# Kernel optimization log

Hardware: AMD Instinct MI355X
Metric: run time of the kernel (lower is better)

The kernel has to match this reference:

```python
import jax, jax.numpy as jnp
import numpy as np


def setup_inputs() -> dict:
    key = jax.random.key(0)
    k1, k2, k3, k4 = jax.random.split(key, 4)
    n, L, h = 512, 257, 256
    l = L - 1
    hidden, n_labels = 256, 50
    feat = jax.random.normal(k1, (n, L, h), dtype=jnp.float32)
    heads = jax.random.randint(k2, (n, l), 0, L, dtype=jnp.int64)
    masks = jnp.ones((n, l), dtype=jnp.float32)
    # torch nn.Linear layout: (out_features, in_features); xavier-normal-ish scale
    W1 = jax.random.normal(k3, (hidden, 2 * h), dtype=jnp.float32) * (2.0 / (hidden + 2 * h)) ** 0.5
    b1 = jnp.zeros((hidden,), dtype=jnp.float32)
    W2 = jax.random.normal(k4, (n_labels, hidden), dtype=jnp.float32) * (2.0 / (n_labels + hidden)) ** 0.5
    b2 = jnp.zeros((n_labels,), dtype=jnp.float32)
    return {"feat": feat, "heads": heads, "masks": masks,
            "W1": W1, "b1": b1, "W2": W2, "b2": b2}


def reference(feat, heads, masks, W1, b1, W2, b2):
    # feat: (n, L, h); heads: (n, l) with l = L-1, values in [0, L)
    dependent_f = feat[:, 1:, :]                                   # (n, l, h)
    # head_f[b, i] = feat[b, heads[b, i]]  (the gather)
    head_f = jnp.take_along_axis(feat, heads[:, :, None], axis=1)   # (n, l, h)
    cat_f = jnp.concatenate((dependent_f, head_f), axis=2)          # (n, l, 2h)
    hid = jax.nn.relu(jnp.einsum('nlh,oh->nlo', cat_f, W1) + b1)    # (n, l, hidden); dropout is identity at eval
    label_f = jnp.einsum('nlo,ko->nlk', hid, W2) + b2               # (n, l, n_labels)
    return label_f
```

## Files before the change

kernel.cpp:

```cpp
#include <hip/hip_runtime.h>
#include <hip/hip_bf16.h>
#include <stdint.h>

typedef __bf16 bf16x8 __attribute__((ext_vector_type(8)));
typedef __bf16 bf16x4 __attribute__((ext_vector_type(4)));
typedef float  floatx4 __attribute__((ext_vector_type(4)));

static constexpr int LL   = 257;
static constexpr int HH   = 256;
static constexpr int M    = 131072;
static constexpr int K1   = 512;
static constexpr int NLAB = 50;

__device__ __forceinline__ bf16x8 cvt8(floatx4 a, floatx4 b) {
  bf16x8 v;
  v[0]=(__bf16)a[0]; v[1]=(__bf16)a[1]; v[2]=(__bf16)a[2]; v[3]=(__bf16)a[3];
  v[4]=(__bf16)b[0]; v[5]=(__bf16)b[1]; v[6]=(__bf16)b[2]; v[7]=(__bf16)b[3];
  return v;
}

__global__ void prep_w(const float* __restrict__ W1, const float* __restrict__ W2,
                       __bf16* __restrict__ w1bt, __bf16* __restrict__ w2b) {
  int idx = blockIdx.x * 256 + threadIdx.x;
  if (idx < 16384) {
    int o  = idx >> 6;
    int kc = idx & 63;
    const float4* s = (const float4*)(W1 + (size_t)o * K1 + kc * 8);
    float4 a = s[0], b = s[1];
    bf16x8 v;
    v[0]=(__bf16)a.x; v[1]=(__bf16)a.y; v[2]=(__bf16)a.z; v[3]=(__bf16)a.w;
    v[4]=(__bf16)b.x; v[5]=(__bf16)b.y; v[6]=(__bf16)b.z; v[7]=(__bf16)b.w;
    *(bf16x8*)(w1bt + ((size_t)(kc * 256 + o)) * 8) = v;
  } else {
    int j = idx - 16384;
    int row = j >> 5;
    int col = (j & 31) * 8;
    float4 a = {0.f,0.f,0.f,0.f}, b = {0.f,0.f,0.f,0.f};
    if (row < NLAB) {
      const float4* s = (const float4*)(W2 + (size_t)row * 256 + col);
      a = s[0]; b = s[1];
    }
    bf16x8 v;
    v[0]=(__bf16)a.x; v[1]=(__bf16)a.y; v[2]=(__bf16)a.z; v[3]=(__bf16)a.w;
    v[4]=(__bf16)b.x; v[5]=(__bf16)b.y; v[6]=(__bf16)b.z; v[7]=(__bf16)b.w;
    *(bf16x8*)(w2b + (size_t)j * 8) = v;
  }
}

template<int KT>
__device__ __forceinline__ void kstep(
    bf16x8 (&afc)[4], bf16x8 (&afi)[4], floatx4 (&acc)[4][4],
    const __bf16* afBase, const __bf16* catS, int bbOff) {

  if constexpr (KT < 14) {
    const __bf16* afp = afBase + (KT + 2) * 8192;
    #pragma unroll
    for (int oi = 0; oi < 4; ++oi)
      afi[oi] = *(const bf16x8*)(afp + oi * 128);
  }

  const __bf16* crd = catS + KT * 2048 + bbOff;
  bf16x8 bb[4];
  #pragma unroll
  for (int mi = 0; mi < 4; ++mi)
    bb[mi] = *(const bf16x8*)(crd + mi * 512);
  #pragma unroll
  for (int oi = 0; oi < 4; ++oi)
    #pragma unroll
    for (int mi = 0; mi < 4; ++mi)
      acc[oi][mi] = __builtin_amdgcn_mfma_f32_16x16x32_bf16(afc[oi], bb[mi], acc[oi][mi], 0, 0, 0);
}

__global__ __launch_bounds__(256, 2)
void fused_kernel(const float* __restrict__ feat, const int* __restrict__ heads,
                  const __bf16* __restrict__ w1bt, const float* __restrict__ b1,
                  const __bf16* __restrict__ w2b, const float* __restrict__ b2,
                  float* __restrict__ out) {
  __shared__ __align__(16) char smem[65536];
  __bf16* catS = (__bf16*)smem;
  __bf16* hidS = (__bf16*)smem;

  const int t    = threadIdx.x;
  const int w    = t >> 6;
  const int lane = t & 63;
  const int lr   = lane & 15;
  const int q    = lane >> 4;

  const int mBase = blockIdx.x * 64;

  const int inrow   = t & 7;
  const int rowslot = t >> 3;
  const int seq     = mBase >> 8;
  const int mA      = mBase + rowslot;
  const int mB      = mBase + 32 + rowslot;
  const float* rp[4];
  rp[0] = feat + ((size_t)(seq * LL + (mA & 255) + 1)) * HH + inrow * 8;
  rp[1] = feat + ((size_t)(seq * LL + (mB & 255) + 1)) * HH + inrow * 8;
  rp[2] = feat + ((size_t)(seq * LL + heads[mA])) * HH + inrow * 8;
  rp[3] = feat + ((size_t)(seq * LL + heads[mB])) * HH + inrow * 8;

  #pragma unroll
  for (int g = 0; g < 4; ++g) {
    const int r = (g & 1) * 32 + rowslot;
    const int kbase = (g >= 2) ? 32 : 0;
    #pragma unroll
    for (int s = 0; s < 4; ++s) {
      floatx4 a = *(const floatx4*)(rp[g] + s * 64);
      floatx4 b = *(const floatx4*)(rp[g] + s * 64 + 4);
      const int ko  = kbase + s * 8 + inrow;
      const int kt  = ko >> 2;
      const int c   = ko & 3;
      const int pos = r * 4 + (c ^ ((r >> 1) & 3));
      *(bf16x8*)(catS + kt * 2048 + pos * 8) = cvt8(a, b);
    }
  }

  const int bbOff = lr * 32 + (q ^ ((lr >> 1) & 3)) * 8;
  const __bf16* afBase = w1bt + ((size_t)(q * 256 + w * 64 + lr)) * 8;

  floatx4 acc[4][4];
  #pragma unroll
  for (int i = 0; i < 4; ++i)
    #pragma unroll
    for (int j = 0; j < 4; ++j)
      acc[i][j] = (floatx4){0.f, 0.f, 0.f, 0.f};

  bf16x8 a0[4], a1[4], a2[4];
  #pragma unroll
  for (int oi = 0; oi < 4; ++oi) a0[oi] = *(const bf16x8*)(afBase + oi * 128);
  #pragma unroll
  for (int oi = 0; oi < 4; ++oi) a1[oi] = *(const bf16x8*)(afBase + 8192 + oi * 128);

  __syncthreads();

  kstep< 0>(a0, a2, acc, afBase, catS, bbOff);
  kstep< 1>(a1, a0, acc, afBase, catS, bbOff);
  kstep< 2>(a2, a1, acc, afBase, catS, bbOff);
  kstep< 3>(a0, a2, acc, afBase, catS, bbOff);
  kstep< 4>(a1, a0, acc, afBase, catS, bbOff);
  kstep< 5>(a2, a1, acc, afBase, catS, bbOff);
  kstep< 6>(a0, a2, acc, afBase, catS, bbOff);
  kstep< 7>(a1, a0, acc, afBase, catS, bbOff);
  kstep< 8>(a2, a1, acc, afBase, catS, bbOff);
  kstep< 9>(a0, a2, acc, afBase, catS, bbOff);
  kstep<10>(a1, a0, acc, afBase, catS, bbOff);
  kstep<11>(a2, a1, acc, afBase, catS, bbOff);
  kstep<12>(a0, a2, acc, afBase, catS, bbOff);
  kstep<13>(a1, a0, acc, afBase, catS, bbOff);
  kstep<14>(a2, a1, acc, afBase, catS, bbOff);
  kstep<15>(a0, a2, acc, afBase, catS, bbOff);

  __syncthreads();

  float4 biasv[4];
  #pragma unroll
  for (int oi = 0; oi < 4; ++oi)
    biasv[oi] = *(const float4*)(b1 + w * 64 + oi * 16 + q * 4);

  #pragma unroll
  for (int mi = 0; mi < 4; ++mi) {
    const int mr = mi * 16 + lr;
    const int s  = lr & 7;
    #pragma unroll
    for (int oi = 0; oi < 4; ++oi) {
      const int cj = w * 8 + oi * 2 + (q >> 1);
      bf16x4 hv;
      const float* bp = (const float*)&biasv[oi];
      #pragma unroll
      for (int rr = 0; rr < 4; ++rr) {
        float v = acc[oi][mi][rr] + bp[rr];
        v = v > 0.f ? v : 0.f;
        hv[rr] = (__bf16)v;
      }
      *(bf16x4*)(hidS + mr * 256 + ((cj ^ s) << 3) + (q & 1) * 4) = hv;
    }
  }
  __syncthreads();

  bf16x8 w2f[8];
  #pragma unroll
  for (int kt2 = 0; kt2 < 8; ++kt2)
    w2f[kt2] = *(const bf16x8*)(w2b + (size_t)(w * 16 + lr) * 256 + kt2 * 32 + q * 8);

  floatx4 acc2[4];
  #pragma unroll
  for (int i = 0; i < 4; ++i) acc2[i] = (floatx4){0.f, 0.f, 0.f, 0.f};

  #pragma unroll
  for (int kt2 = 0; kt2 < 8; ++kt2) {
    const int gc = kt2 * 4 + q;
    #pragma unroll
    for (int mi = 0; mi < 4; ++mi) {
      bf16x8 a2f = *(const bf16x8*)(hidS + (mi * 16 + lr) * 256 + ((gc ^ (lr & 7)) << 3));
      acc2[mi] = __builtin_amdgcn_mfma_f32_16x16x32_bf16(a2f, w2f[kt2], acc2[mi], 0, 0, 0);
    }
  }
  __syncthreads();

  float* outT = (float*)smem;
  const int col = w * 16 + lr;
  if (col < NLAB) {
    const float bias = b2[col];
    #pragma unroll
    for (int mi = 0; mi < 4; ++mi) {
      const int rowB = mi * 16 + q * 4;
      #pragma unroll
      for (int rr = 0; rr < 4; ++rr)
        outT[(rowB + rr) * NLAB + col] = acc2[mi][rr] + bias;
    }
  }
  __syncthreads();

  float* odst = out + (size_t)mBase * NLAB;
  #pragma unroll
  for (int i = t; i < 800; i += 256)
    *(float4*)(odst + i * 4) = *(const float4*)(outT + i * 4);
}

extern "C" void kernel_launch(void* const* d_in, const int* in_sizes, int n_in,
                              void* d_out, int out_size, void* d_ws, size_t ws_size,
                              hipStream_t stream) {
  const float* feat  = (const float*)d_in[0];
  const int*   heads = (const int*)d_in[1];
  const float* W1 = (const float*)d_in[3];
  const float* b1 = (const float*)d_in[4];
  const float* W2 = (const float*)d_in[5];
  const float* b2 = (const float*)d_in[6];
  float* out = (float*)d_out;

  __bf16* w1bt = (__bf16*)d_ws;
  __bf16* w2b  = w1bt + 256 * 512;

  prep_w<<<72, 256, 0, stream>>>(W1, W2, w1bt, w2b);
  fused_kernel<<<M / 64, 256, 0, stream>>>(feat, heads, w1bt, b1, w2b, b2, out);
}
```

Before: 248.9 us.

## Load feature rows straight into registers instead of staging through LDS

Drops the shared-memory staging of the concatenated dependent/head feature tile. Each wave now loads its MFMA B-operand rows directly from global memory as fp32, double-buffered one k-step ahead, and converts them to bf16 in registers. This removes the LDS write/read round trip and one barrier, and halves the shared-memory allocation. The cost is that all four waves re-fetch the same feature rows through the cache with narrower per-row accesses, and register pressure rises from the two fp32 buffers.

Result: slower. 353.3 us (+42.0%).

```diff
diff --git a/kernel.cpp b/kernel.cpp
--- a/kernel.cpp
+++ b/kernel.cpp
@@ -49,9 +49,21 @@
 
 template<int KT>
 __device__ __forceinline__ void kstep(
-    bf16x8 (&afc)[4], bf16x8 (&afi)[4], floatx4 (&acc)[4][4],
-    const __bf16* afBase, const __bf16* catS, int bbOff) {
-
+    floatx4 (&bbc)[8], floatx4 (&bbn)[8],
+    bf16x8 (&afc)[4], bf16x8 (&afi)[4],
+    floatx4 (&acc)[4][4],
+    const float* const (&dp)[4], const float* const (&hp)[4],
+    const __bf16* afBase) {
+
+  if constexpr (KT < 15) {
+    constexpr int CT = KT + 1;
+    #pragma unroll
+    for (int mi = 0; mi < 4; ++mi) {
+      const float* p = (CT < 8) ? (dp[mi] + CT * 32) : (hp[mi] + (CT - 8) * 32);
+      bbn[mi * 2]     = *(const floatx4*)p;
+      bbn[mi * 2 + 1] = *(const floatx4*)(p + 4);
+    }
+  }
   if constexpr (KT < 14) {
     const __bf16* afp = afBase + (KT + 2) * 8192;
     #pragma unroll
@@ -59,11 +71,10 @@
       afi[oi] = *(const bf16x8*)(afp + oi * 128);
   }
 
-  const __bf16* crd = catS + KT * 2048 + bbOff;
   bf16x8 bb[4];
   #pragma unroll
   for (int mi = 0; mi < 4; ++mi)
-    bb[mi] = *(const bf16x8*)(crd + mi * 512);
+    bb[mi] = cvt8(bbc[mi * 2], bbc[mi * 2 + 1]);
   #pragma unroll
   for (int oi = 0; oi < 4; ++oi)
     #pragma unroll
@@ -76,8 +87,7 @@
                   const __bf16* __restrict__ w1bt, const float* __restrict__ b1,
                   const __bf16* __restrict__ w2b, const float* __restrict__ b2,
                   float* __restrict__ out) {
-  __shared__ __align__(16) char smem[65536];
-  __bf16* catS = (__bf16*)smem;
+  __shared__ __align__(16) char smem[32768];
   __bf16* hidS = (__bf16*)smem;
 
   const int t    = threadIdx.x;
@@ -85,37 +95,20 @@
   const int lane = t & 63;
   const int lr   = lane & 15;
   const int q    = lane >> 4;
-
   const int mBase = blockIdx.x * 64;
 
-  const int inrow   = t & 7;
-  const int rowslot = t >> 3;
-  const int seq     = mBase >> 8;
-  const int mA      = mBase + rowslot;
-  const int mB      = mBase + 32 + rowslot;
-  const float* rp[4];
-  rp[0] = feat + ((size_t)(seq * LL + (mA & 255) + 1)) * HH + inrow * 8;
-  rp[1] = feat + ((size_t)(seq * LL + (mB & 255) + 1)) * HH + inrow * 8;
-  rp[2] = feat + ((size_t)(seq * LL + heads[mA])) * HH + inrow * 8;
-  rp[3] = feat + ((size_t)(seq * LL + heads[mB])) * HH + inrow * 8;
-
-  #pragma unroll
-  for (int g = 0; g < 4; ++g) {
-    const int r = (g & 1) * 32 + rowslot;
-    const int kbase = (g >= 2) ? 32 : 0;
-    #pragma unroll
-    for (int s = 0; s < 4; ++s) {
-      floatx4 a = *(const floatx4*)(rp[g] + s * 64);
-      floatx4 b = *(const floatx4*)(rp[g] + s * 64 + 4);
-      const int ko  = kbase + s * 8 + inrow;
-      const int kt  = ko >> 2;
-      const int c   = ko & 3;
-      const int pos = r * 4 + (c ^ ((r >> 1) & 3));
-      *(bf16x8*)(catS + kt * 2048 + pos * 8) = cvt8(a, b);
-    }
-  }
-
-  const int bbOff = lr * 32 + (q ^ ((lr >> 1) & 3)) * 8;
+  const int seq    = mBase >> 8;
+  const int inseq0 = mBase & 255;
+
+  const float* dp[4];
+  const float* hp[4];
+  #pragma unroll
+  for (int mi = 0; mi < 4; ++mi) {
+    const int mrow = mi * 16 + lr;
+    dp[mi] = feat + ((size_t)(seq * LL + inseq0 + mrow + 1)) * HH + q * 8;
+    hp[mi] = feat + ((size_t)(seq * LL + heads[mBase + mrow])) * HH + q * 8;
+  }
+
   const __bf16* afBase = w1bt + ((size_t)(q * 256 + w * 64 + lr)) * 8;
 
   floatx4 acc[4][4];
@@ -125,32 +118,34 @@
     for (int j = 0; j < 4; ++j)
       acc[i][j] = (floatx4){0.f, 0.f, 0.f, 0.f};
 
+  floatx4 bbX[8], bbY[8];
   bf16x8 a0[4], a1[4], a2[4];
   #pragma unroll
+  for (int mi = 0; mi < 4; ++mi) {
+    bbX[mi * 2]     = *(const floatx4*)(dp[mi]);
+    bbX[mi * 2 + 1] = *(const floatx4*)(dp[mi] + 4);
+  }
+  #pragma unroll
   for (int oi = 0; oi < 4; ++oi) a0[oi] = *(const bf16x8*)(afBase + oi * 128);
   #pragma unroll
   for (int oi = 0; oi < 4; ++oi) a1[oi] = *(const bf16x8*)(afBase + 8192 + oi * 128);
 
-  __syncthreads();
-
-  kstep< 0>(a0, a2, acc, afBase, catS, bbOff);
-  kstep< 1>(a1, a0, acc, afBase, catS, bbOff);
-  kstep< 2>(a2, a1, acc, afBase, catS, bbOff);
-  kstep< 3>(a0, a2, acc, afBase, catS, bbOff);
-  kstep< 4>(a1, a0, acc, afBase, catS, bbOff);
-  kstep< 5>(a2, a1, acc, afBase, catS, bbOff);
-  kstep< 6>(a0, a2, acc, afBase, catS, bbOff);
-  kstep< 7>(a1, a0, acc, afBase, catS, bbOff);
-  kstep< 8>(a2, a1, acc, afBase, catS, bbOff);
-  kstep< 9>(a0, a2, acc, afBase, catS, bbOff);
-  kstep<10>(a1, a0, acc, afBase, catS, bbOff);
-  kstep<11>(a2, a1, acc, afBase, catS, bbOff);
-  kstep<12>(a0, a2, acc, afBase, catS, bbOff);
-  kstep<13>(a1, a0, acc, afBase, catS, bbOff);
-  kstep<14>(a2, a1, acc, afBase, catS, bbOff);
-  kstep<15>(a0, a2, acc, afBase, catS, bbOff);
-
-  __syncthreads();
+  kstep< 0>(bbX, bbY, a0, a2, acc, dp, hp, afBase);
+  kstep< 1>(bbY, bbX, a1, a0, acc, dp, hp, afBase);
+  kstep< 2>(bbX, bbY, a2, a1, acc, dp, hp, afBase);
+  kstep< 3>(bbY, bbX, a0, a2, acc, dp, hp, afBase);
+  kstep< 4>(bbX, bbY, a1, a0, acc, dp, hp, afBase);
+  kstep< 5>(bbY, bbX, a2, a1, acc, dp, hp, afBase);
+  kstep< 6>(bbX, bbY, a0, a2, acc, dp, hp, afBase);
+  kstep< 7>(bbY, bbX, a1, a0, acc, dp, hp, afBase);
+  kstep< 8>(bbX, bbY, a2, a1, acc, dp, hp, afBase);
+  kstep< 9>(bbY, bbX, a0, a2, acc, dp, hp, afBase);
+  kstep<10>(bbX, bbY, a1, a0, acc, dp, hp, afBase);
+  kstep<11>(bbY, bbX, a2, a1, acc, dp, hp, afBase);
+  kstep<12>(bbX, bbY, a0, a2, acc, dp, hp, afBase);
+  kstep<13>(bbY, bbX, a1, a0, acc, dp, hp, afBase);
+  kstep<14>(bbX, bbY, a2, a1, acc, dp, hp, afBase);
+  kstep<15>(bbY, bbX, a0, a2, acc, dp, hp, afBase);
 
   float4 biasv[4];
   #pragma unroll
```
